# Kernel tuning notes

Hardware: AMD Instinct MI355X
Metric: run time of the kernel (lower is better)

The kernel has to match this reference:

```python
import jax, jax.numpy as jnp
import numpy as np

MOMENTUM_DECAY = 0.9
AMP_THRESHOLD = 0.1
CORR_THRESHOLD = 0.3
MAX_STEERING = 0.5
EPS = 1e-12  # torch F.normalize eps


def _normalize(x):
    return x / jnp.maximum(jnp.linalg.norm(x), EPS)


def setup_inputs() -> dict:
    key = jax.random.key(0)
    k1, k2, k3 = jax.random.split(key, 3)
    B, S, D = 1, 8192, 4096
    return {
        "hidden_states": jax.random.normal(k1, (B, S, D), dtype=jnp.float32),
        "correct_direction": jax.random.normal(k2, (D,), dtype=jnp.float32),
        "incorrect_direction": jax.random.normal(k3, (D,), dtype=jnp.float32),
        "steering_scale": jnp.ones((1,), dtype=jnp.float32),
    }


def reference(hidden_states, correct_direction, incorrect_direction, steering_scale):
    B, S, D = hidden_states.shape
    # reasoning quality: cosine sims of pooled state against reference directions
    current = hidden_states.mean(axis=1)[0]              # [D] (batch assumed 1)
    current_norm = _normalize(current)
    csim = jnp.where(jnp.linalg.norm(correct_direction) > 0,
                     jnp.dot(current_norm, correct_direction), 0.0)
    isim = jnp.where(jnp.linalg.norm(incorrect_direction) > 0,
                     jnp.dot(current_norm, incorrect_direction), 0.0)
    quality = csim - isim
    steering_dir = _normalize(correct_direction - incorrect_direction)
    # fresh state: momentum_vector is None -> momentum = steering_dir
    momentum = steering_dir
    # adaptive alpha (piecewise in quality)
    amp_alpha = MAX_STEERING * (AMP_THRESHOLD - quality) / (AMP_THRESHOLD + CORR_THRESHOLD)
    alpha = jnp.where(quality < -CORR_THRESHOLD, MAX_STEERING,
                      jnp.where(quality < AMP_THRESHOLD, amp_alpha, 0.05))
    # vectorized per-position steering (replaces the Python for-loop)
    rel_pos = jnp.arange(S, dtype=hidden_states.dtype) / S     # [S]
    pos_weight = 0.5 + 0.5 * rel_pos                           # [S]
    eff_alpha = alpha * pos_weight * steering_scale[0]         # [S]
    delta = eff_alpha[:, None] * momentum[None, :]             # [S, D]
    dnorm = jnp.linalg.norm(delta, axis=-1, keepdims=True)     # [S, 1]
    delta = jnp.where(dnorm > MAX_STEERING, delta * (MAX_STEERING / dnorm), delta)
    return hidden_states + delta[None, :, :]
```

## Files before the change

kernel.cpp:

```cpp
#include <hip/hip_runtime.h>
#include <math.h>

#define EPSV 1e-12f

__global__ __launch_bounds__(256)
void ara_colsum(const float* __restrict__ hid, float* __restrict__ partial,
                int D4, int S, int rows_per_chunk) {
    int d4 = blockIdx.x * 256 + threadIdx.x;
    if (d4 >= D4) return;
    int c = blockIdx.y;
    const float4* h4 = reinterpret_cast<const float4*>(hid);
    float4* p4 = reinterpret_cast<float4*>(partial);
    long row0 = (long)c * rows_per_chunk;
    float4 acc = make_float4(0.f, 0.f, 0.f, 0.f);
#pragma unroll 8
    for (int r = 0; r < rows_per_chunk; ++r) {
        long row = row0 + r;
        if (row < S) {
            float4 v = h4[row * (long)D4 + d4];
            acc.x += v.x; acc.y += v.y; acc.z += v.z; acc.w += v.w;
        }
    }
    p4[(long)c * D4 + d4] = acc;
}

__global__ __launch_bounds__(256)
void ara_reduce(const float* __restrict__ partial, const float* __restrict__ cdir,
                const float* __restrict__ idir, float* __restrict__ ws6,
                int D4, int C) {
    const float4* p4 = reinterpret_cast<const float4*>(partial);
    const float4* c4p = reinterpret_cast<const float4*>(cdir);
    const float4* i4p = reinterpret_cast<const float4*>(idir);
    int lane = threadIdx.x & 63;
    int g = threadIdx.x >> 6;
    int col = blockIdx.x * 64 + lane;
    bool valid = col < D4;
    int per = (C + 3) / 4;
    float4 acc = make_float4(0.f, 0.f, 0.f, 0.f);
    if (valid) {
        for (int j = 0; j < per; ++j) {
            int c = g * per + j;
            if (c < C) {
                float4 v = p4[(long)c * D4 + col];
                acc.x += v.x; acc.y += v.y; acc.z += v.z; acc.w += v.w;
            }
        }
    }
    __shared__ float4 lds[4][64];
    lds[g][lane] = acc;
    __syncthreads();
    if (threadIdx.x < 64) {
        float vals[6] = {0.f, 0.f, 0.f, 0.f, 0.f, 0.f};
        if (valid) {
            float4 s;
            s.x = lds[0][lane].x + lds[1][lane].x + lds[2][lane].x + lds[3][lane].x;
            s.y = lds[0][lane].y + lds[1][lane].y + lds[2][lane].y + lds[3][lane].y;
            s.z = lds[0][lane].z + lds[1][lane].z + lds[2][lane].z + lds[3][lane].z;
            s.w = lds[0][lane].w + lds[1][lane].w + lds[2][lane].w + lds[3][lane].w;
            float4 c = c4p[col], iv = i4p[col];
            vals[0] = c.x*c.x + c.y*c.y + c.z*c.z + c.w*c.w;
            vals[1] = iv.x*iv.x + iv.y*iv.y + iv.z*iv.z + iv.w*iv.w;
            vals[2] = s.x*c.x + s.y*c.y + s.z*c.z + s.w*c.w;
            vals[3] = s.x*iv.x + s.y*iv.y + s.z*iv.z + s.w*iv.w;
            vals[4] = s.x*s.x + s.y*s.y + s.z*s.z + s.w*s.w;
            float dx = c.x-iv.x, dy = c.y-iv.y, dz = c.z-iv.z, dw = c.w-iv.w;
            vals[5] = dx*dx + dy*dy + dz*dz + dw*dw;
        }
#pragma unroll
        for (int k = 0; k < 6; ++k) {
            float v = vals[k];
#pragma unroll
            for (int o = 32; o > 0; o >>= 1) v += __shfl_down(v, o, 64);
            if (lane == 0) ws6[blockIdx.x * 6 + k] = v;
        }
    }
}

__global__ __launch_bounds__(256)
void ara_apply(const float* __restrict__ hid, const float* __restrict__ cdir,
               const float* __restrict__ idir, const float* __restrict__ sscale,
               const float* __restrict__ ws6, float* __restrict__ out,
               int D4, int S, int NB, int rows_per_block) {
    __shared__ float lds[256];
    __shared__ float bc[3];
    int tid = threadIdx.x;
    int n6 = NB * 6;
    if (tid < n6 && tid < 256) lds[tid] = ws6[tid];
    __syncthreads();
    if (tid == 0) {
        float t[6] = {0.f, 0.f, 0.f, 0.f, 0.f, 0.f};
        for (int b = 0; b < NB; ++b)
#pragma unroll
            for (int k = 0; k < 6; ++k) t[k] += lds[b * 6 + k];
        float invS = 1.0f / (float)S;
        float cn = sqrtf(t[4]) * invS;
        float inv_cn = 1.0f / fmaxf(cn, EPSV);
        float csim = (sqrtf(t[0]) > 0.f) ? (t[2] * invS * inv_cn) : 0.f;
        float isim = (sqrtf(t[1]) > 0.f) ? (t[3] * invS * inv_cn) : 0.f;
        float quality = csim - isim;
        float amp = 0.5f * (0.1f - quality) / (0.1f + 0.3f);
        float alpha = (quality < -0.3f) ? 0.5f : ((quality < 0.1f) ? amp : 0.05f);
        float ndiff = sqrtf(t[5]);
        float inv_nd = 1.0f / fmaxf(ndiff, EPSV);
        bc[0] = alpha * sscale[0];
        bc[1] = inv_nd;
        bc[2] = ndiff * inv_nd;
    }
    __syncthreads();
    const float a_s = bc[0], inv_nd = bc[1], mnorm = bc[2];
    const float invS = 1.0f / (float)S;

    const float4* h4 = reinterpret_cast<const float4*>(hid);
    const float4* c4p = reinterpret_cast<const float4*>(cdir);
    const float4* i4p = reinterpret_cast<const float4*>(idir);
    float4* o4 = reinterpret_cast<float4*>(out);

    int jn = D4 >> 8;
    float4 mv[4];
    bool cached = (jn <= 4);
    for (int j = 0; j < jn && j < 4; ++j) {
        int d4 = (j << 8) + tid;
        float4 c = c4p[d4], iv = i4p[d4];
        mv[j].x = (c.x - iv.x) * inv_nd;
        mv[j].y = (c.y - iv.y) * inv_nd;
        mv[j].z = (c.z - iv.z) * inv_nd;
        mv[j].w = (c.w - iv.w) * inv_nd;
    }
    long row0 = (long)blockIdx.x * rows_per_block;
    for (int r = 0; r < rows_per_block; ++r) {
        long s = row0 + r;
        if (s >= S) break;
        float eff = a_s * (0.5f + 0.5f * ((float)s * invS));
        float dn = fabsf(eff) * mnorm;
        float coef = (dn > 0.5f) ? (eff * (0.5f / dn)) : eff;
        for (int j = 0; j < jn; ++j) {
            long idx = s * (long)D4 + (j << 8) + tid;
            float4 m;
            if (cached) {
                m = mv[j];
            } else {
                int d4 = (j << 8) + tid;
                float4 c = c4p[d4], iv = i4p[d4];
                m.x = (c.x - iv.x) * inv_nd; m.y = (c.y - iv.y) * inv_nd;
                m.z = (c.z - iv.z) * inv_nd; m.w = (c.w - iv.w) * inv_nd;
            }
            float4 h = h4[idx];
            float4 rr;
            rr.x = h.x + coef * m.x;
            rr.y = h.y + coef * m.y;
            rr.z = h.z + coef * m.z;
            rr.w = h.w + coef * m.w;
            o4[idx] = rr;
        }
    }
}

extern "C" void kernel_launch(void* const* d_in, const int* in_sizes, int n_in,
                              void* d_out, int out_size, void* d_ws, size_t ws_size,
                              hipStream_t stream) {
    const float* hid    = (const float*)d_in[0];
    const float* cdir   = (const float*)d_in[1];
    const float* idir   = (const float*)d_in[2];
    const float* sscale = (const float*)d_in[3];
    float* out = (float*)d_out;

    int D = in_sizes[1];
    long total = (long)in_sizes[0];
    int S = (int)(total / D);
    int D4 = D / 4;

    const int C = 128;
    int rows_per_chunk = (S + C - 1) / C;

    float* partial = (float*)d_ws;
    float* ws6 = partial + (size_t)C * D;

    dim3 g1((D4 + 255) / 256, C);
    ara_colsum<<<g1, 256, 0, stream>>>(hid, partial, D4, S, rows_per_chunk);

    int NB = (D4 + 63) / 64;
    ara_reduce<<<NB, 256, 0, stream>>>(partial, cdir, idir, ws6, D4, C);

    int rows_per_block = 4;
    int g3 = (S + rows_per_block - 1) / rows_per_block;
    ara_apply<<<g3, 256, 0, stream>>>(hid, cdir, idir, sscale, ws6, out,
                                      D4, S, NB, rows_per_block);
}
```

Before: 98.16 us.

## Fuse column-sum and reduce kernels using last-block atomic counter

Merges the partial column-sum and the cross-chunk reduction into one kernel: each block writes its partial, bumps a per-strip atomic counter, and the last block for a strip sums all partials and computes the six dot/norm terms. This removes one kernel launch and its dependency gap, at the cost of a memset launch, threadfence, and serialized final reduction in a few blocks. The apply kernel now reads the per-strip results directly from global memory instead of staging them in LDS, and rows per block drop from 4 to 2 for more blocks.

```diff
diff --git a/kernel.cpp b/kernel.cpp
--- a/kernel.cpp
+++ b/kernel.cpp
@@ -4,75 +4,78 @@
 #define EPSV 1e-12f
 
 __global__ __launch_bounds__(256)
-void ara_colsum(const float* __restrict__ hid, float* __restrict__ partial,
-                int D4, int S, int rows_per_chunk) {
-    int d4 = blockIdx.x * 256 + threadIdx.x;
-    if (d4 >= D4) return;
-    int c = blockIdx.y;
+void ara_colsum_reduce(const float* __restrict__ hid, const float* __restrict__ cdir,
+                       const float* __restrict__ idir, float* __restrict__ partial,
+                       unsigned int* __restrict__ counters, float* __restrict__ ws6,
+                       int D4, int S, int C, int rows_per_chunk) {
+    const int tid = threadIdx.x;
+    const int strip = blockIdx.x;
+    const int c = blockIdx.y;
+    const int d4 = strip * 256 + tid;
+    const bool valid = (d4 < D4);
+
     const float4* h4 = reinterpret_cast<const float4*>(hid);
     float4* p4 = reinterpret_cast<float4*>(partial);
-    long row0 = (long)c * rows_per_chunk;
-    float4 acc = make_float4(0.f, 0.f, 0.f, 0.f);
-#pragma unroll 8
-    for (int r = 0; r < rows_per_chunk; ++r) {
-        long row = row0 + r;
-        if (row < S) {
-            float4 v = h4[row * (long)D4 + d4];
-            acc.x += v.x; acc.y += v.y; acc.z += v.z; acc.w += v.w;
-        }
-    }
-    p4[(long)c * D4 + d4] = acc;
-}
 
-__global__ __launch_bounds__(256)
-void ara_reduce(const float* __restrict__ partial, const float* __restrict__ cdir,
-                const float* __restrict__ idir, float* __restrict__ ws6,
-                int D4, int C) {
-    const float4* p4 = reinterpret_cast<const float4*>(partial);
-    const float4* c4p = reinterpret_cast<const float4*>(cdir);
-    const float4* i4p = reinterpret_cast<const float4*>(idir);
-    int lane = threadIdx.x & 63;
-    int g = threadIdx.x >> 6;
-    int col = blockIdx.x * 64 + lane;
-    bool valid = col < D4;
-    int per = (C + 3) / 4;
-    float4 acc = make_float4(0.f, 0.f, 0.f, 0.f);
     if (valid) {
-        for (int j = 0; j < per; ++j) {
-            int c = g * per + j;
-            if (c < C) {
-                float4 v = p4[(long)c * D4 + col];
+        long row0 = (long)c * rows_per_chunk;
+        float4 acc = make_float4(0.f, 0.f, 0.f, 0.f);
+#pragma unroll 16
+        for (int r = 0; r < rows_per_chunk; ++r) {
+            long row = row0 + r;
+            if (row < S) {
+                float4 v = h4[row * (long)D4 + d4];
                 acc.x += v.x; acc.y += v.y; acc.z += v.z; acc.w += v.w;
             }
         }
+        p4[(long)c * D4 + d4] = acc;
     }
-    __shared__ float4 lds[4][64];
-    lds[g][lane] = acc;
+    __threadfence();
     __syncthreads();
-    if (threadIdx.x < 64) {
-        float vals[6] = {0.f, 0.f, 0.f, 0.f, 0.f, 0.f};
-        if (valid) {
-            float4 s;
-            s.x = lds[0][lane].x + lds[1][lane].x + lds[2][lane].x + lds[3][lane].x;
-            s.y = lds[0][lane].y + lds[1][lane].y + lds[2][lane].y + lds[3][lane].y;
-            s.z = lds[0][lane].z + lds[1][lane].z + lds[2][lane].z + lds[3][lane].z;
-            s.w = lds[0][lane].w + lds[1][lane].w + lds[2][lane].w + lds[3][lane].w;
-            float4 c = c4p[col], iv = i4p[col];
-            vals[0] = c.x*c.x + c.y*c.y + c.z*c.z + c.w*c.w;
-            vals[1] = iv.x*iv.x + iv.y*iv.y + iv.z*iv.z + iv.w*iv.w;
-            vals[2] = s.x*c.x + s.y*c.y + s.z*c.z + s.w*c.w;
-            vals[3] = s.x*iv.x + s.y*iv.y + s.z*iv.z + s.w*iv.w;
-            vals[4] = s.x*s.x + s.y*s.y + s.z*s.z + s.w*s.w;
-            float dx = c.x-iv.x, dy = c.y-iv.y, dz = c.z-iv.z, dw = c.w-iv.w;
-            vals[5] = dx*dx + dy*dy + dz*dz + dw*dw;
+
+    __shared__ bool is_last;
+    if (tid == 0) {
+        unsigned int old = atomicAdd(&counters[strip], 1u);
+        is_last = (old == (unsigned int)(C - 1));
+    }
+    __syncthreads();
+    if (!is_last) return;
+
+    float4 s = make_float4(0.f, 0.f, 0.f, 0.f);
+    if (valid) {
+        for (int c2 = 0; c2 < C; ++c2) {
+            float4 v = p4[(long)c2 * D4 + d4];
+            s.x += v.x; s.y += v.y; s.z += v.z; s.w += v.w;
         }
+    }
+    float vals[6] = {0.f, 0.f, 0.f, 0.f, 0.f, 0.f};
+    if (valid) {
+        const float4* c4p = reinterpret_cast<const float4*>(cdir);
+        const float4* i4p = reinterpret_cast<const float4*>(idir);
+        float4 cv = c4p[d4], iv = i4p[d4];
+        vals[0] = cv.x*cv.x + cv.y*cv.y + cv.z*cv.z + cv.w*cv.w;
+        vals[1] = iv.x*iv.x + iv.y*iv.y + iv.z*iv.z + iv.w*iv.w;
+        vals[2] = s.x*cv.x + s.y*cv.y + s.z*cv.z + s.w*cv.w;
+        vals[3] = s.x*iv.x + s.y*iv.y + s.z*iv.z + s.w*iv.w;
+        vals[4] = s.x*s.x + s.y*s.y + s.z*s.z + s.w*s.w;
+        float dx = cv.x-iv.x, dy = cv.y-iv.y, dz = cv.z-iv.z, dw = cv.w-iv.w;
+        vals[5] = dx*dx + dy*dy + dz*dz + dw*dw;
+    }
+    __shared__ float red[6][4];
+    int lane = tid & 63;
+    int wid = tid >> 6;
 #pragma unroll
-        for (int k = 0; k < 6; ++k) {
-            float v = vals[k];
+    for (int k = 0; k < 6; ++k) {
+        float v = vals[k];
 #pragma unroll
-            for (int o = 32; o > 0; o >>= 1) v += __shfl_down(v, o, 64);
-            if (lane == 0) ws6[blockIdx.x * 6 + k] = v;
-        }
+        for (int o = 32; o > 0; o >>= 1) v += __shfl_down(v, o, 64);
+        if (lane == 0) red[k][wid] = v;
+    }
+    __syncthreads();
+    if (tid == 0) {
+#pragma unroll
+        for (int k = 0; k < 6; ++k)
+            ws6[strip * 6 + k] = red[k][0] + red[k][1] + red[k][2] + red[k][3];
     }
 }
 
@@ -80,18 +83,14 @@
 void ara_apply(const float* __restrict__ hid, const float* __restrict__ cdir,
                const float* __restrict__ idir, const float* __restrict__ sscale,
                const float* __restrict__ ws6, float* __restrict__ out,
-               int D4, int S, int NB, int rows_per_block) {
-    __shared__ float lds[256];
+               int D4, int S, int NX, int rows_per_block) {
     __shared__ float bc[3];
     int tid = threadIdx.x;
-    int n6 = NB * 6;
-    if (tid < n6 && tid < 256) lds[tid] = ws6[tid];
-    __syncthreads();
     if (tid == 0) {
         float t[6] = {0.f, 0.f, 0.f, 0.f, 0.f, 0.f};
-        for (int b = 0; b < NB; ++b)
+        for (int b = 0; b < NX; ++b)
 #pragma unroll
-            for (int k = 0; k < 6; ++k) t[k] += lds[b * 6 + k];
+            for (int k = 0; k < 6; ++k) t[k] += ws6[b * 6 + k];
         float invS = 1.0f / (float)S;
         float cn = sqrtf(t[4]) * invS;
         float inv_cn = 1.0f / fmaxf(cn, EPSV);
@@ -168,21 +167,23 @@
     long total = (long)in_sizes[0];
     int S = (int)(total / D);
     int D4 = D / 4;
+    int NX = (D4 + 255) / 256;
 
     const int C = 128;
     int rows_per_chunk = (S + C - 1) / C;
 
     float* partial = (float*)d_ws;
-    float* ws6 = partial + (size_t)C * D;
+    unsigned int* counters = (unsigned int*)(partial + (size_t)C * D);
+    float* ws6 = (float*)(counters + NX);
 
-    dim3 g1((D4 + 255) / 256, C);
-    ara_colsum<<<g1, 256, 0, stream>>>(hid, partial, D4, S, rows_per_chunk);
+    hipMemsetAsync(counters, 0, NX * sizeof(unsigned int), stream);
 
-    int NB = (D4 + 63) / 64;
-    ara_reduce<<<NB, 256, 0, stream>>>(partial, cdir, idir, ws6, D4, C);
+    dim3 g1(NX, C);
+    ara_colsum_reduce<<<g1, 256, 0, stream>>>(hid, cdir, idir, partial,
+                                              counters, ws6, D4, S, C, rows_per_chunk);
 
-    int rows_per_block = 4;
+    int rows_per_block = 2;
     int g3 = (S + rows_per_block - 1) / rows_per_block;
     ara_apply<<<g3, 256, 0, stream>>>(hid, cdir, idir, sscale, ws6, out,
-                                      D4, S, NB, rows_per_block);
+                                      D4, S, NX, rows_per_block);
 }
```

After: 176.8 us. +80.1%, slower.
